# Kernel tuning notes

Measured on AMD Instinct MI355X. Metric: run time of the kernel, lower is better.

The kernel has to match this reference:

```python
import jax, jax.numpy as jnp
import numpy as np

N_NODES = 50000
IN_CH = 128
HIDDEN = 64
OUT = 32
HEADS = 4


def _gat_conv(x, src, dst, W, a_src, a_dst, b, heads, ch, concat):
    """PyG-style GATConv (eval mode, self-loops already in src/dst)."""
    N = x.shape[0]
    h = (x @ W).reshape(N, heads, ch)                      # [N,H,C]
    asrc = jnp.einsum('nhc,hc->nh', h, a_src)              # [N,H]
    adst = jnp.einsum('nhc,hc->nh', h, a_dst)              # [N,H]
    e = jax.nn.leaky_relu(asrc[src] + adst[dst], 0.2)      # [E,H]
    # segment softmax over edges grouped by destination node
    m = jax.ops.segment_max(e, dst, num_segments=N)        # [N,H]
    e = jnp.exp(e - m[dst])
    z = jax.ops.segment_sum(e, dst, num_segments=N)        # [N,H]
    alpha = e / (z[dst] + 1e-16)                           # [E,H]
    out = jax.ops.segment_sum(h[src] * alpha[:, :, None], dst, num_segments=N)  # [N,H,C]
    out = out.reshape(N, heads * ch) if concat else out.mean(axis=1)
    return out + b


def _layer_norm(x, g, b):
    mu = x.mean(axis=-1, keepdims=True)
    var = ((x - mu) ** 2).mean(axis=-1, keepdims=True)
    return (x - mu) * jax.lax.rsqrt(var + 1e-5) * g + b


def setup_inputs() -> dict:
    key = jax.random.key(0)
    ks = jax.random.split(key, 20)
    HID = HEADS * HIDDEN  # 256
    s = 0.1
    inp = {
        'x': jax.random.normal(ks[0], (N_NODES, IN_CH), jnp.float32),
        'edge_index': jax.random.randint(ks[1], (2, 800000), 0, N_NODES, jnp.int64 if jax.config.jax_enable_x64 else jnp.int32),
        # conv1
        'W1': jax.random.normal(ks[2], (IN_CH, HID), jnp.float32) * s,
        'a1_src': jax.random.normal(ks[3], (HEADS, HIDDEN), jnp.float32) * s,
        'a1_dst': jax.random.normal(ks[4], (HEADS, HIDDEN), jnp.float32) * s,
        'b1': jnp.zeros((HID,), jnp.float32),
        'g1': jnp.ones((HID,), jnp.float32),
        'be1': jnp.zeros((HID,), jnp.float32),
        # conv2
        'W2': jax.random.normal(ks[5], (HID, HID), jnp.float32) * s,
        'a2_src': jax.random.normal(ks[6], (HEADS, HIDDEN), jnp.float32) * s,
        'a2_dst': jax.random.normal(ks[7], (HEADS, HIDDEN), jnp.float32) * s,
        'b2': jnp.zeros((HID,), jnp.float32),
        'g2': jnp.ones((HID,), jnp.float32),
        'be2': jnp.zeros((HID,), jnp.float32),
        # conv3 (heads=1)
        'W3': jax.random.normal(ks[8], (HID, OUT), jnp.float32) * s,
        'a3_src': jax.random.normal(ks[9], (1, OUT), jnp.float32) * s,
        'a3_dst': jax.random.normal(ks[10], (1, OUT), jnp.float32) * s,
        'b3': jnp.zeros((OUT,), jnp.float32),
    }
    return inp


def reference(x, edge_index, W1, a1_src, a1_dst, b1, g1, be1,
              W2, a2_src, a2_dst, b2, g2, be2,
              W3, a3_src, a3_dst, b3):
    N = x.shape[0]
    loops = jnp.arange(N, dtype=edge_index.dtype)
    ei = jnp.concatenate([edge_index, jnp.stack([loops, loops])], axis=1)
    src, dst = ei[0], ei[1]
    h = _gat_conv(x, src, dst, W1, a1_src, a1_dst, b1, HEADS, HIDDEN, True)
    h = jax.nn.elu(_layer_norm(h, g1, be1))
    h = _gat_conv(h, src, dst, W2, a2_src, a2_dst, b2, HEADS, HIDDEN, True)
    h = jax.nn.elu(_layer_norm(h, g2, be2))
    return _gat_conv(h, src, dst, W3, a3_src, a3_dst, b3, 1, OUT, True)
```

## Files before the change

kernel.cpp:

```cpp
#include <hip/hip_runtime.h>
#include <math.h>

#define NN 50000

typedef __attribute__((ext_vector_type(8))) short bf16x8;
typedef __attribute__((ext_vector_type(4))) float f32x4;

__device__ inline float wred_max(float v){
  #pragma unroll
  for(int s=32;s>0;s>>=1) v=fmaxf(v,__shfl_xor(v,s,64));
  return v;
}
__device__ inline float wred_sum(float v){
  #pragma unroll
  for(int s=32;s>0;s>>=1) v+=__shfl_xor(v,s,64);
  return v;
}
__device__ inline float lrelu(float x){ return x>0.f? x : 0.2f*x; }
__device__ inline float rlf(float v,int l){ return __int_as_float(__builtin_amdgcn_readlane(__float_as_int(v),l)); }

__device__ inline ushort f2bf(float f){
  union{float f;unsigned u;} v; v.f=f;
  unsigned u=v.u;
  return (ushort)((u + 0x7fffu + ((u>>16)&1u)) >> 16);
}
__device__ inline float bflo(unsigned u){ return __uint_as_float(u<<16); }
__device__ inline float bfhi(unsigned u){ return __uint_as_float(u&0xffff0000u); }

__global__ void casttr_k(const float* __restrict__ W, ushort* __restrict__ Wt, int K, int N){
  int i=blockIdx.x*blockDim.x+threadIdx.x;
  if(i<K*N){ int k=i/N, n=i%N; Wt[n*K+k]=f2bf(W[i]); }
}

__global__ void hist_k(const int* __restrict__ dstA,int* __restrict__ counts,int E){
  int i=blockIdx.x*blockDim.x+threadIdx.x;
  if(i<E) atomicAdd(&counts[dstA[i]],1);
}

__global__ __launch_bounds__(1024) void scan1_k(const int* __restrict__ counts,int* __restrict__ offs,
                                                int* __restrict__ bsum,int N){
  __shared__ int stot[16];
  int t=threadIdx.x; int lane=t&63, wv=t>>6;
  int base=blockIdx.x*1024;
  int orig=(base+t<N)?counts[base+t]:0;
  int v=orig;
  #pragma unroll
  for(int s=1;s<64;s<<=1){ int u=__shfl_up(v,s,64); if(lane>=s) v+=u; }
  if(lane==63) stot[wv]=v;
  __syncthreads();
  if(wv==0){
    int tv=(lane<16)?stot[lane]:0;
    #pragma unroll
    for(int s=1;s<16;s<<=1){ int u=__shfl_up(tv,s,64); if(lane>=s) tv+=u; }
    if(lane<16) stot[lane]=tv;
  }
  __syncthreads();
  int wpref=(wv>0)?stot[wv-1]:0;
  if(base+t<N) offs[base+t]=wpref+v-orig;
  if(t==1023) bsum[blockIdx.x]=stot[15];
}
__global__ __launch_bounds__(1024) void scan3_k(int* __restrict__ offs,const int* __restrict__ bsum,int N,int E){
  __shared__ int sbase;
  int t=threadIdx.x;
  if(t<64){
    int v=(t<(int)blockIdx.x)?bsum[t]:0;
    #pragma unroll
    for(int s=32;s>0;s>>=1) v+=__shfl_xor(v,s,64);
    if(t==0) sbase=v;
  }
  __syncthreads();
  int i=blockIdx.x*1024+t;
  if(i<N) offs[i]+=sbase;
  if(i==N-1) offs[N]=E;
}

__global__ void scatter_k(const int* __restrict__ srcA,const int* __restrict__ dstA,
                          const int* __restrict__ offs,int* cur,int* __restrict__ ssrc,int E){
  int i=blockIdx.x*blockDim.x+threadIdx.x;
  if(i<E){ int d=dstA[i]; int p=offs[d]+atomicAdd(&cur[d],1); ssrc[p]=srcA[i]; }
}

template<int WR,int WC,int MI,int NI,int DOTM,int AF32>
__global__ __launch_bounds__(256,2) void gemm_bf16_k(const void* __restrict__ Av,
    const ushort* __restrict__ Bt, ushort* __restrict__ C,
    const float* __restrict__ aS, const float* __restrict__ aD,
    float* __restrict__ as_, float* __restrict__ ad_,
    int M, int N, int K){
  constexpr int BM = WR*MI*16;
  constexpr int BN = WC*NI*16;
  constexpr int LDK = 40;
  __shared__ ushort sA[BM*LDK];
  __shared__ ushort sB[BN*LDK];
  int tid=threadIdx.x;
  int lane=tid&63, w=tid>>6;
  int wr=w/WC, wc=w%WC;
  int bm=blockIdx.y*BM, bn=blockIdx.x*BN;
  f32x4 acc[MI][NI]={};

  for(int k0=0;k0<K;k0+=32){
    if constexpr (AF32){
      const float* A=(const float*)Av;
      #pragma unroll
      for(int i=0;i<(BM*8)/256;i++){
        int c=tid+i*256;
        int r=c>>3, cc=c&7;
        int gr=bm+r;
        float4 v={0.f,0.f,0.f,0.f};
        if(gr<M) v=*(const float4*)(A+(size_t)gr*K+k0+cc*4);
        unsigned long long p=(unsigned long long)f2bf(v.x)
          |((unsigned long long)f2bf(v.y)<<16)
          |((unsigned long long)f2bf(v.z)<<32)
          |((unsigned long long)f2bf(v.w)<<48);
        *(unsigned long long*)(sA+r*LDK+cc*4)=p;
      }
    } else {
      const ushort* A=(const ushort*)Av;
      #pragma unroll
      for(int i=0;i<(BM*4)/256;i++){
        int c=tid+i*256;
        int r=c>>2, cc=c&3;
        int gr=bm+r;
        ulonglong2 v; v.x=0; v.y=0;
        if(gr<M) v=*(const ulonglong2*)(A+(size_t)gr*K+k0+cc*8);
        *(ulonglong2*)(sA+r*LDK+cc*8)=v;
      }
    }
    if constexpr ((BN*4)>=256){
      #pragma unroll
      for(int i=0;i<(BN*4)/256;i++){
        int c=tid+i*256;
        int r=c>>2, cc=c&3;
        ulonglong2 v=*(const ulonglong2*)(Bt+(size_t)(bn+r)*K+k0+cc*8);
        *(ulonglong2*)(sB+r*LDK+cc*8)=v;
      }
    } else {
      if(tid<BN*4){
        int r=tid>>2, cc=tid&3;
        ulonglong2 v=*(const ulonglong2*)(Bt+(size_t)(bn+r)*K+k0+cc*8);
        *(ulonglong2*)(sB+r*LDK+cc*8)=v;
      }
    }
    __syncthreads();
    bf16x8 af[MI], bf[NI];
    #pragma unroll
    for(int m=0;m<MI;m++)
      af[m]=*(bf16x8*)(sA+((wr*MI+m)*16+(lane&15))*LDK+(lane>>4)*8);
    #pragma unroll
    for(int n=0;n<NI;n++)
      bf[n]=*(bf16x8*)(sB+((wc*NI+n)*16+(lane&15))*LDK+(lane>>4)*8);
    #pragma unroll
    for(int m=0;m<MI;m++)
      #pragma unroll
      for(int n=0;n<NI;n++)
        acc[m][n]=__builtin_amdgcn_mfma_f32_16x16x32_bf16(af[m],bf[n],acc[m][n],0,0,0);
    __syncthreads();
  }
  int rb=lane>>4, cl=lane&15;
  float av[NI], dv[NI];
  #pragma unroll
  for(int n=0;n<NI;n++){
    int gc=bn+(wc*NI+n)*16+cl;
    if constexpr (DOTM!=0){ av[n]=aS[gc]; dv[n]=aD[gc]; }
    else { av[n]=0.f; dv[n]=0.f; }
  }
  #pragma unroll
  for(int m=0;m<MI;m++){
    #pragma unroll
    for(int i=0;i<4;i++){
      int gr=bm+(wr*MI+m)*16+rb*4+i;
      if constexpr (DOTM==1){
        int h=(bn>>6)+wc;
        float ps=0.f,pd=0.f;
        #pragma unroll
        for(int n=0;n<NI;n++){ ps+=acc[m][n][i]*av[n]; pd+=acc[m][n][i]*dv[n]; }
        #pragma unroll
        for(int msk=1;msk<16;msk<<=1){
          ps+=__shfl_xor(ps,msk,64); pd+=__shfl_xor(pd,msk,64);
        }
        if(cl==0 && gr<M){ as_[gr*4+h]=ps; ad_[gr*4+h]=pd; }
      } else if constexpr (DOTM==2){
        float ps=0.f,pd=0.f;
        #pragma unroll
        for(int n=0;n<NI;n++){ ps+=acc[m][n][i]*av[n]; pd+=acc[m][n][i]*dv[n]; }
        #pragma unroll
        for(int msk=1;msk<16;msk<<=1){
          ps+=__shfl_xor(ps,msk,64); pd+=__shfl_xor(pd,msk,64);
        }
        if(cl==0 && gr<M){ as_[gr]=ps; ad_[gr]=pd; }
      }
      if(gr<M){
        #pragma unroll
        for(int n=0;n<NI;n++){
          int gc=bn+(wc*NI+n)*16+cl;
          int pos = (DOTM==1) ? (4*(gc&63)+(gc>>6)) : gc;
          C[(size_t)gr*N+pos]=f2bf(acc[m][n][i]);
        }
      }
    }
  }
}

__global__ __launch_bounds__(256) void agg4_k(const ushort* __restrict__ hb,
    const float* __restrict__ as_,const float* __restrict__ ad_,
    const int* __restrict__ offs,const int* __restrict__ ssrc,
    const float* __restrict__ bias,const float* __restrict__ g,const float* __restrict__ be,
    ushort* __restrict__ outb,int N){
  __shared__ float wlds[4][64][4];
  int lane=threadIdx.x&63, wv=threadIdx.x>>6;
  int n=blockIdx.x*4+wv; if(n>=N) return;
  int lane4=lane*4;
  float ad[4], es[4];
  #pragma unroll
  for(int k=0;k<4;k++) ad[k]=ad_[n*4+k];
  #pragma unroll
  for(int k=0;k<4;k++) es[k]=lrelu(as_[n*4+k]+ad[k]);
  int o0=offs[n],o1=offs[n+1];
  int cnt=o1-o0;
  float m[4], inv[4], acc[4];

  if(cnt<=64){
    int sv=0;
    float lv[4]={-1e30f,-1e30f,-1e30f,-1e30f};
    if(lane<cnt){
      sv=ssrc[o0+lane];
      float4 avv=*(const float4*)(as_+(size_t)sv*4);
      lv[0]=lrelu(avv.x+ad[0]); lv[1]=lrelu(avv.y+ad[1]);
      lv[2]=lrelu(avv.z+ad[2]); lv[3]=lrelu(avv.w+ad[3]);
    }
    #pragma unroll
    for(int k=0;k<4;k++) m[k]=fmaxf(es[k],wred_max(lv[k]));
    float w4[4];
    #pragma unroll
    for(int k=0;k<4;k++) w4[k]=(lane<cnt)?__expf(lv[k]-m[k]):0.f;
    #pragma unroll
    for(int k=0;k<4;k++){
      float z=wred_sum(w4[k])+__expf(es[k]-m[k]);
      inv[k]=1.f/(z+1e-16f);
    }
    #pragma unroll
    for(int k=0;k<4;k++) w4[k]*=inv[k];
    *(float4*)&wlds[wv][lane][0]=make_float4(w4[0],w4[1],w4[2],w4[3]);
    asm volatile("s_waitcnt lgkmcnt(0)":::"memory");
    {
      uint2 u=*(const uint2*)(hb+(size_t)n*256+lane4);
      float hv[4]={bflo(u.x),bfhi(u.x),bflo(u.y),bfhi(u.y)};
      #pragma unroll
      for(int k=0;k<4;k++) acc[k]=__expf(es[k]-m[k])*inv[k]*hv[k];
    }
    int nbat=(cnt+7)>>3;
    for(int b=0;b<nbat;b++){
      int e0=b*8;
      uint2 u[8];
      #pragma unroll
      for(int i=0;i<8;i++){
        int s=__builtin_amdgcn_readlane(sv,e0+i);
        u[i]=*(const uint2*)(hb+((size_t)s<<8)+lane4);
      }
      #pragma unroll
      for(int i=0;i<8;i++){
        const float* wp=&wlds[wv][e0+i][0];
        acc[0]+=wp[0]*bflo(u[i].x);
        acc[1]+=wp[1]*bfhi(u[i].x);
        acc[2]+=wp[2]*bflo(u[i].y);
        acc[3]+=wp[3]*bfhi(u[i].y);
      }
    }
  } else {
    #pragma unroll
    for(int k=0;k<4;k++) m[k]=es[k];
    {
      float lm[4]={-1e30f,-1e30f,-1e30f,-1e30f};
      for(int j=o0+lane;j<o1;j+=64){
        int s=ssrc[j];
        float4 avv=*(const float4*)(as_+(size_t)s*4);
        float a[4]={avv.x,avv.y,avv.z,avv.w};
        #pragma unroll
        for(int k=0;k<4;k++) lm[k]=fmaxf(lm[k],lrelu(a[k]+ad[k]));
      }
      #pragma unroll
      for(int k=0;k<4;k++) m[k]=fmaxf(m[k],wred_max(lm[k]));
    }
    {
      float lz[4]={0.f,0.f,0.f,0.f};
      for(int j=o0+lane;j<o1;j+=64){
        int s=ssrc[j];
        float4 avv=*(const float4*)(as_+(size_t)s*4);
        float a[4]={avv.x,avv.y,avv.z,avv.w};
        #pragma unroll
        for(int k=0;k<4;k++) lz[k]+=__expf(lrelu(a[k]+ad[k])-m[k]);
      }
      #pragma unroll
      for(int k=0;k<4;k++){
        float z=wred_sum(lz[k])+__expf(es[k]-m[k]);
        inv[k]=1.f/(z+1e-16f);
      }
    }
    {
      uint2 u=*(const uint2*)(hb+(size_t)n*256+lane4);
      float hv[4]={bflo(u.x),bfhi(u.x),bflo(u.y),bfhi(u.y)};
      #pragma unroll
      for(int k=0;k<4;k++) acc[k]=__expf(es[k]-m[k])*inv[k]*hv[k];
    }
    for(int base=o0;base<o1;base+=64){
      int c2=min(64,o1-base);
      int j=base+lane;
      int sv=0; float w4[4]={0.f,0.f,0.f,0.f};
      if(j<o1){
        sv=ssrc[j];
        float4 avv=*(const float4*)(as_+(size_t)sv*4);
        float a[4]={avv.x,avv.y,avv.z,avv.w};
        #pragma unroll
        for(int k=0;k<4;k++) w4[k]=__expf(lrelu(a[k]+ad[k])-m[k])*inv[k];
      }
      for(int t=0;t<c2;t++){
        int s=__builtin_amdgcn_readlane(sv,t);
        uint2 u=*(const uint2*)(hb+(size_t)s*256+lane4);
        acc[0]+=rlf(w4[0],t)*bflo(u.x);
        acc[1]+=rlf(w4[1],t)*bfhi(u.x);
        acc[2]+=rlf(w4[2],t)*bflo(u.y);
        acc[3]+=rlf(w4[3],t)*bfhi(u.y);
      }
    }
  }
  #pragma unroll
  for(int k=0;k<4;k++) acc[k]+=bias[k*64+lane];
  float tot=wred_sum(acc[0]+acc[1]+acc[2]+acc[3]);
  float mu=tot*(1.f/256.f);
  float vs=0.f;
  #pragma unroll
  for(int k=0;k<4;k++){ float d=acc[k]-mu; vs+=d*d; }
  float var=wred_sum(vs)*(1.f/256.f);
  float r=rsqrtf(var+1e-5f);
  #pragma unroll
  for(int k=0;k<4;k++){
    float v=(acc[k]-mu)*r*g[k*64+lane]+be[k*64+lane];
    float ev= v>0.f? v : expm1f(v);
    outb[(size_t)n*256+k*64+lane]=f2bf(ev);
  }
}

__global__ __launch_bounds__(256) void agg1_k(const ushort* __restrict__ hb,
    const float* __restrict__ as_,const float* __restrict__ ad_,
    const int* __restrict__ offs,const int* __restrict__ ssrc,
    const float* __restrict__ bias,float* __restrict__ out,int N){
  int lane=threadIdx.x&63, wv=threadIdx.x>>6;
  int n=blockIdx.x*4+wv; if(n>=N) return;
  float ad=ad_[n];
  float es=lrelu(as_[n]+ad);
  int o0=offs[n],o1=offs[n+1];
  int cnt=o1-o0;
  float m, inv, acc=0.f;
  int lane32=lane&31;
  int half=lane>>5;

  if(cnt<=64){
    int sv=0; float lv=-1e30f;
    if(lane<cnt){ sv=ssrc[o0+lane]; lv=lrelu(as_[sv]+ad); }
    m=fmaxf(es,wred_max(lv));
    float w1=(lane<cnt)?__expf(lv-m):0.f;
    float z=wred_sum(w1)+__expf(es-m);
    inv=1.f/(z+1e-16f);
    w1*=inv;
    if(half==0) acc=__expf(es-m)*inv*__uint_as_float(((unsigned)hb[(size_t)n*32+lane32])<<16);
    int cnt2=(cnt+1)&~1;
    for(int t=0;t<cnt2;t+=2){
      int sL=__builtin_amdgcn_readlane(sv,t);
      int sH=__builtin_amdgcn_readlane(sv,t+1);
      float wL=rlf(w1,t), wH=rlf(w1,t+1);
      int s = half? sH : sL;
      float ww = half? wH : wL;
      float hv=__uint_as_float(((unsigned)hb[(size_t)s*32+lane32])<<16);
      acc+=ww*hv;
    }
    acc+=__shfl_xor(acc,32,64);
  } else {
    m=es;
    {
      float lm=-1e30f;
      for(int j=o0+lane;j<o1;j+=64) lm=fmaxf(lm,lrelu(as_[ssrc[j]]+ad));
      m=fmaxf(m,wred_max(lm));
    }
    {
      float lz=0.f;
      for(int j=o0+lane;j<o1;j+=64) lz+=__expf(lrelu(as_[ssrc[j]]+ad)-m);
      float z=wred_sum(lz)+__expf(es-m);
      inv=1.f/(z+1e-16f);
    }
    if(lane<32) acc=__expf(es-m)*inv*__uint_as_float(((unsigned)hb[(size_t)n*32+lane])<<16);
    for(int base=o0;base<o1;base+=64){
      int c2=min(64,o1-base);
      int j=base+lane;
      int sv=0; float w1=0.f;
      if(j<o1){ sv=ssrc[j]; w1=__expf(lrelu(as_[sv]+ad)-m)*inv; }
      for(int t=0;t<c2;t++){
        int s=__builtin_amdgcn_readlane(sv,t);
        if(lane<32) acc+=rlf(w1,t)*__uint_as_float(((unsigned)hb[(size_t)s*32+lane])<<16);
      }
    }
  }
  if(lane<32) out[(size_t)n*32+lane]=acc+bias[lane];
}

extern "C" void kernel_launch(void* const* d_in,const int* in_sizes,int n_in,
                              void* d_out,int out_size,void* d_ws,size_t ws_size,
                              hipStream_t stream){
  const float* x  =(const float*)d_in[0];
  const int*   ei =(const int*)  d_in[1];
  const float* W1 =(const float*)d_in[2];
  const float* a1s=(const float*)d_in[3];
  const float* a1d=(const float*)d_in[4];
  const float* b1 =(const float*)d_in[5];
  const float* g1 =(const float*)d_in[6];
  const float* be1=(const float*)d_in[7];
  const float* W2 =(const float*)d_in[8];
  const float* a2s=(const float*)d_in[9];
  const float* a2d=(const float*)d_in[10];
  const float* b2 =(const float*)d_in[11];
  const float* g2 =(const float*)d_in[12];
  const float* be2=(const float*)d_in[13];
  const float* W3 =(const float*)d_in[14];
  const float* a3s=(const float*)d_in[15];
  const float* a3d=(const float*)d_in[16];
  const float* b3 =(const float*)d_in[17];
  float* outp=(float*)d_out;
  int N=NN;
  int E=in_sizes[1]/2;
  const int* srcA=ei;
  const int* dstA=ei+E;

  char* w=(char*)d_ws;
  ushort* hb =(ushort*)w; w+=(size_t)N*256*2;
  ushort* h3b=(ushort*)w; w+=(size_t)N*32*2;
  ushort* obb=(ushort*)w; w+=(size_t)N*256*2;
  ushort* w1t=(ushort*)w; w+=(size_t)256*128*2;
  ushort* w2t=(ushort*)w; w+=(size_t)256*256*2;
  ushort* w3t=(ushort*)w; w+=(size_t)32*256*2;
  float* asb =(float*)w; w+=(size_t)N*4*4;
  float* adb =(float*)w; w+=(size_t)N*4*4;
  int* offs=(int*)w; w+=(size_t)(N+4)*4;
  int* cur =(int*)w; w+=(size_t)N*4;
  int* ssrc=(int*)w; w+=(size_t)E*4;
  int* bsum=(int*)w; w+=(size_t)64*4;

  int NB=(N+1023)/1024;

  hipMemsetAsync(cur,0,(size_t)N*4,stream);
  hist_k<<<(E+255)/256,256,0,stream>>>(dstA,cur,E);
  scan1_k<<<NB,1024,0,stream>>>(cur,offs,bsum,N);
  scan3_k<<<NB,1024,0,stream>>>(offs,bsum,N,E);
  hipMemsetAsync(cur,0,(size_t)N*4,stream);
  scatter_k<<<(E+255)/256,256,0,stream>>>(srcA,dstA,offs,cur,ssrc,E);

  casttr_k<<<(128*256+255)/256,256,0,stream>>>(W1,w1t,128,256);
  casttr_k<<<(256*256+255)/256,256,0,stream>>>(W2,w2t,256,256);
  casttr_k<<<(256*32+255)/256,256,0,stream>>>(W3,w3t,256,32);

  int nblkN=(N+3)/4;
  int gY128=(N+127)/128;

  gemm_bf16_k<2,2,4,4,1,1><<<dim3(2,gY128),256,0,stream>>>(x,w1t,hb,a1s,a1d,asb,adb,N,256,128);
  agg4_k<<<nblkN,256,0,stream>>>(hb,asb,adb,offs,ssrc,b1,g1,be1,obb,N);

  gemm_bf16_k<2,2,4,4,1,0><<<dim3(2,gY128),256,0,stream>>>(obb,w2t,hb,a2s,a2d,asb,adb,N,256,256);
  agg4_k<<<nblkN,256,0,stream>>>(hb,asb,adb,offs,ssrc,b2,g2,be2,obb,N);

  gemm_bf16_k<4,1,2,2,2,0><<<dim3(1,gY128),256,0,stream>>>(obb,w3t,h3b,a3s,a3d,asb,adb,N,32,256);
  agg1_k<<<nblkN,256,0,stream>>>(h3b,asb,adb,offs,ssrc,b3,outp,N);
}
```

Baseline: 344.8 us.

## Use direct global-to-LDS loads with XOR swizzle and fuse small setup kernels

The GEMM tile loads for bf16 operands now use global_load_lds to copy 16-byte chunks directly into shared memory. Row padding is replaced by an XOR swizzle to avoid bank conflicts, and the fp32 A path loads 8 values per thread. The three weight cast/transpose kernels are merged into one launch, and scan1 zeroes the counts so one memset can be dropped. Together these aim to cut register round-trips and launch overhead, at the cost of more complex addressing and reliance on the exact lane ordering of the direct-LDS copy.

```diff
diff --git a/kernel.cpp b/kernel.cpp
--- a/kernel.cpp
+++ b/kernel.cpp
@@ -27,9 +27,18 @@
 __device__ inline float bflo(unsigned u){ return __uint_as_float(u<<16); }
 __device__ inline float bfhi(unsigned u){ return __uint_as_float(u&0xffff0000u); }
 
-__global__ void casttr_k(const float* __restrict__ W, ushort* __restrict__ Wt, int K, int N){
-  int i=blockIdx.x*blockDim.x+threadIdx.x;
-  if(i<K*N){ int k=i/N, n=i%N; Wt[n*K+k]=f2bf(W[i]); }
+__device__ inline void gload_lds16(const void* g, void* l){
+  __builtin_amdgcn_global_load_lds((const __attribute__((address_space(1))) void*)g,
+                                   (__attribute__((address_space(3))) void*)l, 16, 0, 0);
+}
+
+__global__ void casttr3_k(const float* __restrict__ W1,const float* __restrict__ W2,
+                          const float* __restrict__ W3,
+                          ushort* __restrict__ w1t,ushort* __restrict__ w2t,ushort* __restrict__ w3t){
+  int i=blockIdx.x*256+threadIdx.x;
+  if(i<32768){ int k=i>>8, n=i&255; w1t[n*128+k]=f2bf(W1[i]); }
+  else if(i<98304){ int j=i-32768; int k=j>>8, n=j&255; w2t[n*256+k]=f2bf(W2[j]); }
+  else { int j=i-98304; int k=j>>5, n=j&31; w3t[n*256+k]=f2bf(W3[j]); }
 }
 
 __global__ void hist_k(const int* __restrict__ dstA,int* __restrict__ counts,int E){
@@ -37,7 +46,7 @@
   if(i<E) atomicAdd(&counts[dstA[i]],1);
 }
 
-__global__ __launch_bounds__(1024) void scan1_k(const int* __restrict__ counts,int* __restrict__ offs,
+__global__ __launch_bounds__(1024) void scan1_k(int* __restrict__ counts,int* __restrict__ offs,
                                                 int* __restrict__ bsum,int N){
   __shared__ int stot[16];
   int t=threadIdx.x; int lane=t&63, wv=t>>6;
@@ -56,7 +65,7 @@
   }
   __syncthreads();
   int wpref=(wv>0)?stot[wv-1]:0;
-  if(base+t<N) offs[base+t]=wpref+v-orig;
+  if(base+t<N){ offs[base+t]=wpref+v-orig; counts[base+t]=0; }
   if(t==1023) bsum[blockIdx.x]=stot[15];
 }
 __global__ __launch_bounds__(1024) void scan3_k(int* __restrict__ offs,const int* __restrict__ bsum,int N,int E){
@@ -88,9 +97,8 @@
     int M, int N, int K){
   constexpr int BM = WR*MI*16;
   constexpr int BN = WC*NI*16;
-  constexpr int LDK = 40;
-  __shared__ ushort sA[BM*LDK];
-  __shared__ ushort sB[BN*LDK];
+  __shared__ ushort sA[BM*32];
+  __shared__ ushort sB[BN*32];
   int tid=threadIdx.x;
   int lane=tid&63, w=tid>>6;
   int wr=w/WC, wc=w%WC;
@@ -101,53 +109,57 @@
     if constexpr (AF32){
       const float* A=(const float*)Av;
       #pragma unroll
-      for(int i=0;i<(BM*8)/256;i++){
-        int c=tid+i*256;
-        int r=c>>3, cc=c&7;
-        int gr=bm+r;
-        float4 v={0.f,0.f,0.f,0.f};
-        if(gr<M) v=*(const float4*)(A+(size_t)gr*K+k0+cc*4);
-        unsigned long long p=(unsigned long long)f2bf(v.x)
-          |((unsigned long long)f2bf(v.y)<<16)
-          |((unsigned long long)f2bf(v.z)<<32)
-          |((unsigned long long)f2bf(v.w)<<48);
-        *(unsigned long long*)(sA+r*LDK+cc*4)=p;
+      for(int p=0;p<(BM*4)/256;p++){
+        int idx=tid+p*256;
+        int r=idx>>2, cs=idx&3;
+        int c=cs^(r&3);
+        int gr=min(bm+r,M-1);
+        float4 v0=*(const float4*)(A+(size_t)gr*K+k0+c*8);
+        float4 v1=*(const float4*)(A+(size_t)gr*K+k0+c*8+4);
+        ulonglong2 pk;
+        pk.x=(unsigned long long)f2bf(v0.x)|((unsigned long long)f2bf(v0.y)<<16)
+            |((unsigned long long)f2bf(v0.z)<<32)|((unsigned long long)f2bf(v0.w)<<48);
+        pk.y=(unsigned long long)f2bf(v1.x)|((unsigned long long)f2bf(v1.y)<<16)
+            |((unsigned long long)f2bf(v1.z)<<32)|((unsigned long long)f2bf(v1.w)<<48);
+        *(ulonglong2*)(sA+r*32+cs*8)=pk;
       }
     } else {
       const ushort* A=(const ushort*)Av;
       #pragma unroll
-      for(int i=0;i<(BM*4)/256;i++){
-        int c=tid+i*256;
-        int r=c>>2, cc=c&3;
-        int gr=bm+r;
-        ulonglong2 v; v.x=0; v.y=0;
-        if(gr<M) v=*(const ulonglong2*)(A+(size_t)gr*K+k0+cc*8);
-        *(ulonglong2*)(sA+r*LDK+cc*8)=v;
-      }
-    }
-    if constexpr ((BN*4)>=256){
-      #pragma unroll
-      for(int i=0;i<(BN*4)/256;i++){
-        int c=tid+i*256;
-        int r=c>>2, cc=c&3;
-        ulonglong2 v=*(const ulonglong2*)(Bt+(size_t)(bn+r)*K+k0+cc*8);
-        *(ulonglong2*)(sB+r*LDK+cc*8)=v;
-      }
-    } else {
-      if(tid<BN*4){
-        int r=tid>>2, cc=tid&3;
-        ulonglong2 v=*(const ulonglong2*)(Bt+(size_t)(bn+r)*K+k0+cc*8);
-        *(ulonglong2*)(sB+r*LDK+cc*8)=v;
+      for(int rr=0;rr<2;rr++){
+        int rbase=w*32+rr*16;
+        int r=rbase+(lane>>2);
+        int cs=lane&3;
+        int c=cs^(r&3);
+        int gr=min(bm+r,M-1);
+        gload_lds16(A+(size_t)gr*K+k0+c*8, sA+rbase*32);
+      }
+    }
+    {
+      #pragma unroll
+      for(int i=0;i<(BN/16+3)/4;i++){
+        int ii=w+i*4;
+        if(ii<BN/16){
+          int rbase=ii*16;
+          int r=rbase+(lane>>2);
+          int cs=lane&3;
+          int c=cs^(r&3);
+          gload_lds16(Bt+(size_t)(bn+r)*K+k0+c*8, sB+rbase*32);
+        }
       }
     }
     __syncthreads();
     bf16x8 af[MI], bf[NI];
     #pragma unroll
-    for(int m=0;m<MI;m++)
-      af[m]=*(bf16x8*)(sA+((wr*MI+m)*16+(lane&15))*LDK+(lane>>4)*8);
-    #pragma unroll
-    for(int n=0;n<NI;n++)
-      bf[n]=*(bf16x8*)(sB+((wc*NI+n)*16+(lane&15))*LDK+(lane>>4)*8);
+    for(int m=0;m<MI;m++){
+      int rA=(wr*MI+m)*16+(lane&15);
+      af[m]=*(bf16x8*)(sA+rA*32+(((lane>>4)^(rA&3))*8));
+    }
+    #pragma unroll
+    for(int n=0;n<NI;n++){
+      int rB=(wc*NI+n)*16+(lane&15);
+      bf[n]=*(bf16x8*)(sB+rB*32+(((lane>>4)^(rB&3))*8));
+    }
     #pragma unroll
     for(int m=0;m<MI;m++)
       #pragma unroll
@@ -448,12 +460,9 @@
   hist_k<<<(E+255)/256,256,0,stream>>>(dstA,cur,E);
   scan1_k<<<NB,1024,0,stream>>>(cur,offs,bsum,N);
   scan3_k<<<NB,1024,0,stream>>>(offs,bsum,N,E);
-  hipMemsetAsync(cur,0,(size_t)N*4,stream);
   scatter_k<<<(E+255)/256,256,0,stream>>>(srcA,dstA,offs,cur,ssrc,E);
 
-  casttr_k<<<(128*256+255)/256,256,0,stream>>>(W1,w1t,128,256);
-  casttr_k<<<(256*256+255)/256,256,0,stream>>>(W2,w2t,256,256);
-  casttr_k<<<(256*32+255)/256,256,0,stream>>>(W3,w3t,256,32);
+  casttr3_k<<<416,256,0,stream>>>(W1,W2,W3,w1t,w2t,w3t);
 
   int nblkN=(N+3)/4;
   int gY128=(N+127)/128;
```

Measured after the change: 335.7 us. 2.6% less time.
